# Optimization experiments

Measured on AMD Instinct MI355X. Metric: run time of the kernel, lower is better.

## Reference

```python
import jax, jax.numpy as jnp
import numpy as np

B, T = 32, 2000
H = 512          # hidden_size
NH = 100         # n_harmonics
NM = 65          # n_magnitudes
E = 16           # energy_state dim
HH = 256         # hypernetwork hidden


def _lin_init(k, out_d, in_d):
    return jax.random.normal(k, (out_d, in_d), jnp.float32) / np.sqrt(in_d)


def setup_inputs() -> dict:
    key = jax.random.key(0)
    ks = jax.random.split(key, 24)
    inp = {
        'f0_scaled': jax.random.uniform(ks[0], (B, T), jnp.float32),
        'loudness': jax.random.uniform(ks[1], (B, T), jnp.float32),
        'energy_state': jax.random.normal(ks[2], (B, E), jnp.float32),
        # base decoder params
        'pre_W': _lin_init(ks[3], H, 2), 'pre_b': jnp.zeros((H,), jnp.float32),
        'W_ih': _lin_init(ks[4], 3 * H, H), 'W_hh': _lin_init(ks[5], 3 * H, H),
        'b_ih': jnp.zeros((3 * H,), jnp.float32), 'b_hh': jnp.zeros((3 * H,), jnp.float32),
        'post_W': _lin_init(ks[6], H, H), 'post_b': jnp.zeros((H,), jnp.float32),
        'harm_W': _lin_init(ks[7], NH, H), 'harm_b': jnp.zeros((NH,), jnp.float32),
        'noise_W': _lin_init(ks[8], NM, H), 'noise_b': jnp.zeros((NM,), jnp.float32),
        # hypernetwork params (small output scale so deltas are perturbative)
        'hyp_W1': _lin_init(ks[9], HH, E), 'hyp_b1': jnp.zeros((HH,), jnp.float32),
        'hyp_Wdh': _lin_init(ks[10], NH * H, HH) * 0.05, 'hyp_bdh': jnp.zeros((NH * H,), jnp.float32),
        'hyp_Wbh': _lin_init(ks[11], NH, HH) * 0.05, 'hyp_bbh': jnp.zeros((NH,), jnp.float32),
        'hyp_Wdn': _lin_init(ks[12], NM * H, HH) * 0.05, 'hyp_bdn': jnp.zeros((NM * H,), jnp.float32),
        'hyp_Wbn': _lin_init(ks[13], NM, HH) * 0.05, 'hyp_bbn': jnp.zeros((NM,), jnp.float32),
    }
    return inp


def _gru(x, W_ih, W_hh, b_ih, b_hh):
    # x: [B,T,H] -> [B,T,H], torch nn.GRU cell equations
    gi = jnp.einsum('bth,gh->btg', x, W_ih) + b_ih  # [B,T,3H]
    gi = jnp.swapaxes(gi, 0, 1)  # [T,B,3H]
    h0 = jnp.zeros((x.shape[0], W_hh.shape[1]), x.dtype)

    def step(h, gi_t):
        gh = h @ W_hh.T + b_hh
        ir, iz, in_ = jnp.split(gi_t, 3, axis=-1)
        hr, hz, hn = jnp.split(gh, 3, axis=-1)
        r = jax.nn.sigmoid(ir + hr)
        z = jax.nn.sigmoid(iz + hz)
        n = jnp.tanh(in_ + r * hn)
        h_new = (1.0 - z) * n + z * h
        return h_new, h_new

    _, ys = jax.lax.scan(step, h0, gi)
    return jnp.swapaxes(ys, 0, 1)  # [B,T,H]


def reference(f0_scaled, loudness, energy_state,
              pre_W, pre_b, W_ih, W_hh, b_ih, b_hh, post_W, post_b,
              harm_W, harm_b, noise_W, noise_b,
              hyp_W1, hyp_b1, hyp_Wdh, hyp_bdh, hyp_Wbh, hyp_bbh,
              hyp_Wdn, hyp_bdn, hyp_Wbn, hyp_bbn):
    Bs = energy_state.shape[0]
    # Hypernetwork: energy_state -> per-batch weight/bias deltas
    h = jax.nn.relu(energy_state @ hyp_W1.T + hyp_b1)            # [B,HH]
    dW_harm = (h @ hyp_Wdh.T + hyp_bdh).reshape(Bs, NH, H)
    db_harm = h @ hyp_Wbh.T + hyp_bbh                            # [B,NH]
    dW_noise = (h @ hyp_Wdn.T + hyp_bdn).reshape(Bs, NM, H)
    db_noise = h @ hyp_Wbn.T + hyp_bbn                           # [B,NM]

    # Base decoder trunk
    x = jnp.stack([f0_scaled, loudness], axis=-1)                # [B,T,2]
    x = jax.nn.leaky_relu(jnp.einsum('bti,hi->bth', x, pre_W) + pre_b)
    x = _gru(x, W_ih, W_hh, b_ih, b_hh)
    x = jax.nn.leaky_relu(jnp.einsum('bth,oh->bto', x, post_W) + post_b)

    # Modulated heads: per-batch effective weight shared across T (no [B*T,O,H] blow-up)
    eff_hW = harm_W[None] + dW_harm                              # [B,NH,H]
    eff_hb = harm_b[None] + db_harm                              # [B,NH]
    harm_out = jnp.einsum('bth,boh->bto', x, eff_hW) + eff_hb[:, None, :]
    harmonic_amps = jax.nn.sigmoid(harm_out)                     # [B,T,NH]

    eff_nW = noise_W[None] + dW_noise                            # [B,NM,H]
    eff_nb = noise_b[None] + db_noise                            # [B,NM]
    noise_out = jnp.einsum('bth,boh->bto', x, eff_nW) + eff_nb[:, None, :]
    noise_mags = jax.nn.sigmoid(noise_out)                       # [B,T,NM]
    return harmonic_amps, noise_mags
```

## Files before the change

kernel.cpp:

```cpp
#include <hip/hip_runtime.h>
#include <hip/hip_fp16.h>
#include <stdint.h>

#define B_  32
#define T_  2000
#define H_  512
#define NH_ 100
#define NM_ 65

typedef _Float16 f16x8 __attribute__((ext_vector_type(8)));
typedef _Float16 f16x2 __attribute__((ext_vector_type(2)));
typedef float    f32x4 __attribute__((ext_vector_type(4)));

typedef __attribute__((address_space(3))) void lds_void_t;
typedef __attribute__((address_space(1))) void glb_void_t;

__device__ __forceinline__ void gload_lds16(const void* g, void* l) {
  __builtin_amdgcn_global_load_lds((const glb_void_t*)g, (lds_void_t*)l, 16, 0, 0);
}

__device__ __forceinline__ float sigmoidf_(float x) {
  float e = __builtin_amdgcn_exp2f(-x * 1.44269504f);
  return __builtin_amdgcn_rcpf(1.0f + e);
}
__device__ __forceinline__ float tanhf_(float x) {
  float e = __builtin_amdgcn_exp2f(x * 2.88539008f);
  return 1.0f - 2.0f * __builtin_amdgcn_rcpf(e + 1.0f);
}
__device__ __forceinline__ float dot2(unsigned w, unsigned h, float acc) {
  return __builtin_amdgcn_fdot2(__builtin_bit_cast(f16x2, w),
                                __builtin_bit_cast(f16x2, h), acc, false);
}
__device__ __forceinline__ unsigned pack2(float a, float b) {
  __half2 h = __floats2half2_rn(a, b);
  return __builtin_bit_cast(unsigned, h);
}
__device__ __forceinline__ float hsel(unsigned w, int hi) {
  __half2 h2 = __builtin_bit_cast(__half2, w);
  return hi ? __high2float(h2) : __low2float(h2);
}

__global__ void hyper1(const float* __restrict__ es, const float* __restrict__ W1,
                       const float* __restrict__ b1, float* __restrict__ hE) {
  int b = blockIdx.x, o = threadIdx.x;
  float a = b1[o];
  #pragma unroll
  for (int c = 0; c < 16; ++c) a += es[b*16 + c] * W1[o*16 + c];
  hE[b*256 + o] = fmaxf(a, 0.f);
}

__global__ void hyper2(const float* __restrict__ hE,
                       const float* __restrict__ Wbh, const float* __restrict__ bbh,
                       const float* __restrict__ harmb,
                       const float* __restrict__ Wbn, const float* __restrict__ bbn,
                       const float* __restrict__ noiseb, float* __restrict__ effb) {
  int b = blockIdx.x, o = threadIdx.x;
  if (o < NH_) {
    float a = bbh[o] + harmb[o];
    for (int c = 0; c < 256; ++c) a += hE[b*256 + c] * Wbh[o*256 + c];
    effb[b*256 + o] = a;
  } else if (o < NH_ + NM_) {
    int q = o - NH_;
    float a = bbn[q] + noiseb[q];
    for (int c = 0; c < 256; ++c) a += hE[b*256 + c] * Wbn[q*256 + c];
    effb[b*256 + o] = a;
  }
}

__global__ __launch_bounds__(256) void hyper3(
    const float* __restrict__ hE, const float* __restrict__ Wd,
    const float* __restrict__ bd, const float* __restrict__ baseW,
    __half* __restrict__ effW, int o_base) {
  __shared__ float wl[256*33];
  __shared__ float hEl[32*256];
  int tid = threadIdx.x;
  int row0 = blockIdx.x * 256;
  #pragma unroll
  for (int i = 0; i < 32; ++i) hEl[i*256 + tid] = hE[i*256 + tid];
  float acc[32];
  #pragma unroll
  for (int b = 0; b < 32; ++b) acc[b] = 0.f;
  for (int cc = 0; cc < 256; cc += 32) {
    __syncthreads();
    #pragma unroll
    for (int i = 0; i < 32; ++i) {
      int idx = i*256 + tid;
      int r = idx >> 5, c = idx & 31;
      wl[r*33 + c] = Wd[(size_t)(row0 + r)*256 + cc + c];
    }
    __syncthreads();
    #pragma unroll
    for (int c = 0; c < 32; ++c) {
      float w = wl[tid*33 + c];
      #pragma unroll
      for (int b = 0; b < 32; ++b) acc[b] += w * hEl[b*256 + cc + c];
    }
  }
  int row = row0 + tid;
  int o = row >> 9, h = row & 511;
  float base = baseW[row] + bd[row];
  #pragma unroll
  for (int b = 0; b < 32; ++b) {
    effW[((size_t)b*256 + o_base + o)*512 + h] = (__half)(acc[b] + base);
  }
}

__global__ void cvt_f16(const float* __restrict__ in, __half* __restrict__ out, int n) {
  int i = blockIdx.x*256 + threadIdx.x;
  if (i < n) out[i] = (__half)in[i];
}

__global__ void pack_whh3(const float* __restrict__ Whh, uint4* __restrict__ Wp3) {
  int idx = blockIdx.x*256 + threadIdx.x;
  int t = idx % 384;
  int k = (idx / 384) & 31;
  int w = idx / (384*32);
  int rr = t >> 1, ch = t & 1;
  int g = rr >> 6, j = rr & 63;
  int row = g*512 + w*64 + j;
  int col0 = ch*256 + k*8;
  const float* src = Whh + (size_t)row*512 + col0;
  uint4 o;
  o.x = pack2(src[0], src[1]);
  o.y = pack2(src[2], src[3]);
  o.z = pack2(src[4], src[5]);
  o.w = pack2(src[6], src[7]);
  Wp3[idx] = o;
}

__global__ void pre_kernel(const float* __restrict__ f0, const float* __restrict__ loud,
                           const float* __restrict__ preW, const float* __restrict__ preb,
                           __half* __restrict__ xpre, int CH, int c0) {
  int b = blockIdx.y;
  int idx = blockIdx.x*256 + threadIdx.x;
  int t = idx >> 9, h = idx & 511;
  int mg = b*T_ + c0 + t;
  float v = f0[mg]*preW[h*2+0] + loud[mg]*preW[h*2+1] + preb[h];
  v = v >= 0.f ? v : 0.01f*v;
  xpre[((size_t)b*CH + t)*512 + h] = (__half)v;
}

template<int ACT>
__global__ __launch_bounds__(256) void gemm_nt(
    const __half* __restrict__ A, const __half* __restrict__ B,
    __half* __restrict__ C, const float* __restrict__ bias, int N) {
  constexpr int K = 512;
  __shared__ __align__(16) __half As[128*64];
  __shared__ __align__(16) __half Bs[128*64];
  int tid = threadIdx.x;
  int bx = blockIdx.x, by = blockIdx.y;
  const __half* Ab = A + (size_t)bx*128*K;
  const __half* Bb = B + (size_t)by*128*K;
  f32x4 acc[4][4] = {};
  int lane = tid & 63;
  int wv = tid >> 6, wr = wv >> 1, wc = wv & 1;
  int lr = lane & 15, lk = lane >> 4;

  for (int kt = 0; kt < K/64; ++kt) {
    #pragma unroll
    for (int j = 0; j < 4; ++j) {
      int idx = j*256 + tid;
      int row = idx >> 3, seg = idx & 7;
      const __half* gpA = Ab + (size_t)row*K + kt*64 + seg*8;
      const __half* gpB = Bb + (size_t)row*K + kt*64 + seg*8;
      __half* lpA = As + (size_t)(j*256 + (tid & ~63))*8;
      __half* lpB = Bs + (size_t)(j*256 + (tid & ~63))*8;
      gload_lds16(gpA, lpA);
      gload_lds16(gpB, lpB);
    }
    __syncthreads();
    #pragma unroll
    for (int ks = 0; ks < 2; ++ks) {
      f16x8 af[4], bf[4];
      #pragma unroll
      for (int i = 0; i < 4; ++i)
        af[i] = *(const f16x8*)(As + (wr*64 + i*16 + lr)*64 + ks*32 + lk*8);
      #pragma unroll
      for (int j2 = 0; j2 < 4; ++j2)
        bf[j2] = *(const f16x8*)(Bs + (wc*64 + j2*16 + lr)*64 + ks*32 + lk*8);
      #pragma unroll
      for (int i = 0; i < 4; ++i)
        #pragma unroll
        for (int j2 = 0; j2 < 4; ++j2)
          acc[i][j2] = __builtin_amdgcn_mfma_f32_16x16x32_f16(af[i], bf[j2], acc[i][j2], 0, 0, 0);
    }
    __syncthreads();
  }

  #pragma unroll
  for (int j2 = 0; j2 < 4; ++j2) {
    int col = by*128 + wc*64 + j2*16 + lr;
    float bv = bias[col];
    #pragma unroll
    for (int i = 0; i < 4; ++i) {
      int row0 = bx*128 + wr*64 + i*16 + lk*4;
      #pragma unroll
      for (int r = 0; r < 4; ++r) {
        float v = acc[i][j2][r] + bv;
        if (ACT == 1) v = v >= 0.f ? v : 0.01f*v;
        C[(size_t)(row0 + r)*N + col] = (__half)v;
      }
    }
  }
}

__global__ __launch_bounds__(256) void heads_gemm(
    const __half* __restrict__ Apc, const __half* __restrict__ effW,
    const float* __restrict__ effb, float* __restrict__ out, int CH, int c0) {
  constexpr int K = 512;
  __shared__ __align__(16) __half As[128*64];
  __shared__ __align__(16) __half Bs[128*64];
  int tid = threadIdx.x;
  int bx = blockIdx.x, by = blockIdx.y, b = blockIdx.z;
  const __half* Ab = Apc + (size_t)b*CH*K;
  const __half* Bb = effW + ((size_t)b*256 + (size_t)by*128)*K;
  f32x4 acc[4][4] = {};
  int lane = tid & 63;
  int wv = tid >> 6, wr = wv >> 1, wc = wv & 1;
  int lr = lane & 15, lk = lane >> 4;

  for (int kt = 0; kt < K/64; ++kt) {
    #pragma unroll
    for (int j = 0; j < 4; ++j) {
      int idx = j*256 + tid;
      int row = idx >> 3, seg = idx & 7;
      int ar = bx*128 + row; if (ar > CH-1) ar = CH-1;
      const __half* gpA = Ab + (size_t)ar*K + kt*64 + seg*8;
      const __half* gpB = Bb + (size_t)row*K + kt*64 + seg*8;
      __half* lpA = As + (size_t)(j*256 + (tid & ~63))*8;
      __half* lpB = Bs + (size_t)(j*256 + (tid & ~63))*8;
      gload_lds16(gpA, lpA);
      gload_lds16(gpB, lpB);
    }
    __syncthreads();
    #pragma unroll
    for (int ks = 0; ks < 2; ++ks) {
      f16x8 af[4], bf[4];
      #pragma unroll
      for (int i = 0; i < 4; ++i)
        af[i] = *(const f16x8*)(As + (wr*64 + i*16 + lr)*64 + ks*32 + lk*8);
      #pragma unroll
      for (int j2 = 0; j2 < 4; ++j2)
        bf[j2] = *(const f16x8*)(Bs + (wc*64 + j2*16 + lr)*64 + ks*32 + lk*8);
      #pragma unroll
      for (int i = 0; i < 4; ++i)
        #pragma unroll
        for (int j2 = 0; j2 < 4; ++j2)
          acc[i][j2] = __builtin_amdgcn_mfma_f32_16x16x32_f16(af[i], bf[j2], acc[i][j2], 0, 0, 0);
    }
    __syncthreads();
  }

  #pragma unroll
  for (int j2 = 0; j2 < 4; ++j2) {
    int o = by*128 + wc*64 + j2*16 + lr;
    if (o < NH_ + NM_) {
      float bv = effb[b*256 + o];
      #pragma unroll
      for (int i = 0; i < 4; ++i) {
        #pragma unroll
        for (int r = 0; r < 4; ++r) {
          int trow = bx*128 + wr*64 + i*16 + lk*4 + r;
          if (trow < CH) {
            int tg = c0 + trow;
            float v = sigmoidf_(acc[i][j2][r] + bv);
            if (o < NH_)
              out[((size_t)b*T_ + tg)*NH_ + o] = v;
            else
              out[(size_t)B_*T_*NH_ + ((size_t)b*T_ + tg)*NM_ + (o - NH_)] = v;
          }
        }
      }
    }
  }
}

#define LOADW(k) { const uint4* p = Wp3 + ((size_t)(w*32 + (k)))*384 + t; \
  asm volatile("global_load_dwordx4 %0, %1, off" : "=v"(wq_##k) : "v"(p) : "memory"); }

#define DOTW(k, A) { uint4 hv = *(const uint4*)&hq[ch*132 + (k)*4]; \
  A = dot2(wq_##k.x, hv.x, A); A = dot2(wq_##k.y, hv.y, A); \
  A = dot2(wq_##k.z, hv.z, A); A = dot2(wq_##k.w, hv.w, A); }

__global__ __launch_bounds__(512) __attribute__((amdgpu_waves_per_eu(2, 4)))
void gru_scan8(
    const uint4* __restrict__ Wp3, const __half* __restrict__ gi_c,
    const float* __restrict__ bhh, __half* __restrict__ ys_c,
    float* __restrict__ hstate, unsigned long long* __restrict__ xch64,
    int CH, int first) {
  int wg = blockIdx.x;
  int b = wg & 31;
  int w = wg >> 5;
  int t = threadIdx.x;
  int rr = t >> 1, ch = t & 1;
  bool wact = (t < 384);

  __shared__ __align__(16) unsigned hq[264];
  __shared__ float part[384];
  __shared__ float gil[192];
  __shared__ unsigned sval[32];

  uint4 wq_0{},wq_1{},wq_2{},wq_3{},wq_4{},wq_5{},wq_6{},wq_7{},
        wq_8{},wq_9{},wq_10{},wq_11{},wq_12{},wq_13{},wq_14{},wq_15{},
        wq_16{},wq_17{},wq_18{},wq_19{},wq_20{},wq_21{},wq_22{},wq_23{},
        wq_24{},wq_25{},wq_26{},wq_27{},wq_28{},wq_29{},wq_30{},wq_31{};
  if (wact) {
    LOADW(0)  LOADW(1)  LOADW(2)  LOADW(3)  LOADW(4)  LOADW(5)  LOADW(6)  LOADW(7)
    LOADW(8)  LOADW(9)  LOADW(10) LOADW(11) LOADW(12) LOADW(13) LOADW(14) LOADW(15)
    LOADW(16) LOADW(17) LOADW(18) LOADW(19) LOADW(20) LOADW(21) LOADW(22) LOADW(23)
    LOADW(24) LOADW(25) LOADW(26) LOADW(27) LOADW(28) LOADW(29) LOADW(30) LOADW(31)
  }
  asm volatile("s_waitcnt vmcnt(0)" ::: "memory");
  __builtin_amdgcn_sched_barrier(0);

  float br0=0.f,br1=0.f,bz0=0.f,bz1=0.f,bn0=0.f,bn1=0.f;
  if (t < 32) {
    int u0 = w*64 + 2*t;
    br0 = bhh[u0];        br1 = bhh[u0+1];
    bz0 = bhh[512+u0];    bz1 = bhh[512+u0+1];
    bn0 = bhh[1024+u0];   bn1 = bhh[1024+u0+1];
  }

  if (t < 256) {
    unsigned hv0 = first ? 0u : pack2(hstate[b*512 + 2*t], hstate[b*512 + 2*t + 1]);
    hq[t < 128 ? t : t + 4] = hv0;
  }
  __syncthreads();

  const __half* gib = gi_c + (size_t)b*CH*1536;
  __half* ysb = ys_c + (size_t)b*CH*512;

  for (int s = 0; s < CH; ++s) {
    int p = s & 1;
    unsigned long long* xp64 = xch64 + ((size_t)p*32 + b)*256;
    float giv = 0.f;
    if (t < 192) giv = (float)gib[(size_t)s*1536 + (t >> 6)*512 + w*64 + (t & 63)];

    if (wact) {
      float a0 = 0.f, a1 = 0.f, a2 = 0.f, a3 = 0.f;
      DOTW(0,a0)  DOTW(1,a1)  DOTW(2,a2)  DOTW(3,a3)
      DOTW(4,a0)  DOTW(5,a1)  DOTW(6,a2)  DOTW(7,a3)
      DOTW(8,a0)  DOTW(9,a1)  DOTW(10,a2) DOTW(11,a3)
      DOTW(12,a0) DOTW(13,a1) DOTW(14,a2) DOTW(15,a3)
      DOTW(16,a0) DOTW(17,a1) DOTW(18,a2) DOTW(19,a3)
      DOTW(20,a0) DOTW(21,a1) DOTW(22,a2) DOTW(23,a3)
      DOTW(24,a0) DOTW(25,a1) DOTW(26,a2) DOTW(27,a3)
      DOTW(28,a0) DOTW(29,a1) DOTW(30,a2) DOTW(31,a3)
      part[rr*2 + ch] = (a0 + a1) + (a2 + a3);
      if (t < 192) gil[t] = giv;
    }
    __syncthreads();

    if (t < 32) {
      int j0 = 2*t, j1 = 2*t + 1;
      float ghr0 = part[j0*2] + part[j0*2+1] + br0;
      float ghr1 = part[j1*2] + part[j1*2+1] + br1;
      float ghz0 = part[(64+j0)*2] + part[(64+j0)*2+1] + bz0;
      float ghz1 = part[(64+j1)*2] + part[(64+j1)*2+1] + bz1;
      float ghn0 = part[(128+j0)*2] + part[(128+j0)*2+1] + bn0;
      float ghn1 = part[(128+j1)*2] + part[(128+j1)*2+1] + bn1;
      float r0 = sigmoidf_(gil[j0] + ghr0);
      float r1 = sigmoidf_(gil[j1] + ghr1);
      float z0 = sigmoidf_(gil[64+j0] + ghz0);
      float z1 = sigmoidf_(gil[64+j1] + ghz1);
      float n0 = tanhf_(gil[128+j0] + r0*ghn0);
      float n1 = tanhf_(gil[128+j1] + r1*ghn1);
      int gidx = w*32 + t;
      unsigned hold = hq[gidx < 128 ? gidx : gidx + 4];
      float h0 = (1.f - z0)*n0 + z0*hsel(hold, 0);
      float h1 = (1.f - z1)*n1 + z1*hsel(hold, 1);
      unsigned hv = pack2(h0, h1);
      *(unsigned*)&ysb[(size_t)s*512 + w*64 + j0] = hv;
      unsigned long long tv = ((unsigned long long)(unsigned)(s + 1) << 32)
                              | (unsigned long long)hv;
      __hip_atomic_store(&xp64[w*32 + t], tv,
                         __ATOMIC_RELAXED, __HIP_MEMORY_SCOPE_AGENT);
      sval[t] = hv;
      if (s == CH - 1) {
        hstate[b*512 + w*64 + j0] = h0;
        hstate[b*512 + w*64 + j1] = h1;
      }
    }
    __syncthreads();
    if (t < 256) {
      unsigned hv;
      if ((t >> 5) == w) {
        hv = sval[t & 31];
      } else {
        unsigned long long v;
        do {
          v = __hip_atomic_load(&xp64[t], __ATOMIC_RELAXED, __HIP_MEMORY_SCOPE_AGENT);
        } while ((unsigned)(v >> 32) != (unsigned)(s + 1));
        hv = (unsigned)v;
      }
      hq[t < 128 ? t : t + 4] = hv;
    }
    __syncthreads();
  }
}

extern "C" void kernel_launch(void* const* d_in, const int* in_sizes, int n_in,
                              void* d_out, int out_size, void* d_ws, size_t ws_size,
                              hipStream_t stream) {
  const float* f0     = (const float*)d_in[0];
  const float* loud   = (const float*)d_in[1];
  const float* es     = (const float*)d_in[2];
  const float* preW   = (const float*)d_in[3];
  const float* preb   = (const float*)d_in[4];
  const float* Wih    = (const float*)d_in[5];
  const float* Whh    = (const float*)d_in[6];
  const float* b_ih   = (const float*)d_in[7];
  const float* b_hh   = (const float*)d_in[8];
  const float* postW  = (const float*)d_in[9];
  const float* postb  = (const float*)d_in[10];
  const float* harmW  = (const float*)d_in[11];
  const float* harmb  = (const float*)d_in[12];
  const float* noiseW = (const float*)d_in[13];
  const float* noiseb = (const float*)d_in[14];
  const float* hypW1  = (const float*)d_in[15];
  const float* hypb1  = (const float*)d_in[16];
  const float* Wdh    = (const float*)d_in[17];
  const float* bdh    = (const float*)d_in[18];
  const float* Wbh    = (const float*)d_in[19];
  const float* bbh    = (const float*)d_in[20];
  const float* Wdn    = (const float*)d_in[21];
  const float* bdn    = (const float*)d_in[22];
  const float* Wbn    = (const float*)d_in[23];
  const float* bbn    = (const float*)d_in[24];
  (void)in_sizes; (void)n_in; (void)out_size;

  const size_t FIXED = 13312ull*1024ull;
  int CH = 20;
  {
    const int opts[8] = {2000, 1000, 500, 400, 200, 100, 40, 20};
    for (int i = 0; i < 8; ++i) {
      size_t need = FIXED + (size_t)opts[i] * 163840ull + 65536ull;
      if (need <= ws_size) { CH = opts[i]; break; }
    }
  }
  const int NC = T_ / CH;
  const int Mc = B_ * CH;

  char* w = (char*)d_ws;
  size_t off = 0;
  auto alloc = [&](size_t bytes) -> void* {
    void* p = (void*)(w + off);
    off += (bytes + 255) & ~(size_t)255;
    return p;
  };
  float*    hE      = (float*)alloc((size_t)32*256*4);
  float*    effb    = (float*)alloc((size_t)32*256*4);
  float*    hstate  = (float*)alloc((size_t)32*512*4);
  __half*   effW    = (__half*)alloc((size_t)32*256*512*2);
  __half*   Wih16   = (__half*)alloc((size_t)1536*512*2);
  __half*   postW16 = (__half*)alloc((size_t)512*512*2);
  uint4*    Wp3     = (uint4*)alloc((size_t)8*32*384*16 + 4096);
  unsigned long long* xch64 = (unsigned long long*)alloc((size_t)2*32*256*8);
  __half*   xpre    = (__half*)alloc((size_t)Mc*512*2);
  __half*   gibuf   = (__half*)alloc((size_t)Mc*1536*2);
  __half*   ysbuf   = (__half*)alloc((size_t)Mc*512*2);
  __half*   postc   = xpre;

  hyper1<<<32, 256, 0, stream>>>(es, hypW1, hypb1, hE);
  hyper2<<<32, 256, 0, stream>>>(hE, Wbh, bbh, harmb, Wbn, bbn, noiseb, effb);
  hyper3<<<200, 256, 0, stream>>>(hE, Wdh, bdh, harmW, effW, 0);
  hyper3<<<130, 256, 0, stream>>>(hE, Wdn, bdn, noiseW, effW, NH_);
  cvt_f16<<<(1536*512)/256, 256, 0, stream>>>(Wih, Wih16, 1536*512);
  cvt_f16<<<(512*512)/256, 256, 0, stream>>>(postW, postW16, 512*512);
  pack_whh3<<<384, 256, 0, stream>>>(Whh, Wp3);

  for (int c = 0; c < NC; ++c) {
    int c0 = c * CH;
    pre_kernel<<<dim3(CH*2, 32), 256, 0, stream>>>(f0, loud, preW, preb, xpre, CH, c0);
    gemm_nt<0><<<dim3(Mc/128, 12), 256, 0, stream>>>(xpre, Wih16, gibuf, b_ih, 1536);
    gru_scan8<<<256, 512, 0, stream>>>(Wp3, gibuf, b_hh, ysbuf, hstate, xch64,
                                       CH, c == 0 ? 1 : 0);
    gemm_nt<1><<<dim3(Mc/128, 4), 256, 0, stream>>>(ysbuf, postW16, postc, postb, 512);
    heads_gemm<<<dim3((CH+127)/128, 2, 32), 256, 0, stream>>>(postc, effW, effb,
                                                              (float*)d_out, CH, c0);
  }
}
```

Measured before the change: 4.512 ms.

## Move GRU gate combine to idle wave and cut per-step barriers

The gate-combine step moves from threads 0-31 to an otherwise idle wave (threads 384-415). That wave writes its own new hidden slice straight into hq, while the other threads spin-poll for remote slices at the same time. This removes one of the three block barriers per timestep, and the remaining barriers become raw s_barrier with an lgkmcnt wait. The gi load for the next step is also prefetched one iteration ahead. The change adds a data race risk, because hq is written while other lanes may still read it, and the hand-written barrier depends on correct waitcnt handling.

```diff
diff --git a/kernel.cpp b/kernel.cpp
--- a/kernel.cpp
+++ b/kernel.cpp
@@ -282,6 +282,9 @@
   A = dot2(wq_##k.x, hv.x, A); A = dot2(wq_##k.y, hv.y, A); \
   A = dot2(wq_##k.z, hv.z, A); A = dot2(wq_##k.w, hv.w, A); }
 
+#define BARX() do { asm volatile("s_waitcnt lgkmcnt(0)\n\ts_barrier" ::: "memory"); \
+                    __builtin_amdgcn_sched_barrier(0); } while (0)
+
 __global__ __launch_bounds__(512) __attribute__((amdgpu_waves_per_eu(2, 4)))
 void gru_scan8(
     const uint4* __restrict__ Wp3, const __half* __restrict__ gi_c,
@@ -292,13 +295,14 @@
   int b = wg & 31;
   int w = wg >> 5;
   int t = threadIdx.x;
-  int rr = t >> 1, ch = t & 1;
+  int ch = t & 1;
   bool wact = (t < 384);
+  bool comb = (t >= 384 && t < 416);
+  int tc = t - 384;
 
   __shared__ __align__(16) unsigned hq[264];
   __shared__ float part[384];
   __shared__ float gil[192];
-  __shared__ unsigned sval[32];
 
   uint4 wq_0{},wq_1{},wq_2{},wq_3{},wq_4{},wq_5{},wq_6{},wq_7{},
         wq_8{},wq_9{},wq_10{},wq_11{},wq_12{},wq_13{},wq_14{},wq_15{},
@@ -314,8 +318,8 @@
   __builtin_amdgcn_sched_barrier(0);
 
   float br0=0.f,br1=0.f,bz0=0.f,bz1=0.f,bn0=0.f,bn1=0.f;
-  if (t < 32) {
-    int u0 = w*64 + 2*t;
+  if (comb) {
+    int u0 = w*64 + 2*tc;
     br0 = bhh[u0];        br1 = bhh[u0+1];
     bz0 = bhh[512+u0];    bz1 = bhh[512+u0+1];
     bn0 = bhh[1024+u0];   bn1 = bhh[1024+u0+1];
@@ -330,11 +334,15 @@
   const __half* gib = gi_c + (size_t)b*CH*1536;
   __half* ysb = ys_c + (size_t)b*CH*512;
 
+  float giv_cur = 0.f, giv_next = 0.f;
+  if (t < 192) giv_cur = (float)gib[(t >> 6)*512 + w*64 + (t & 63)];
+
   for (int s = 0; s < CH; ++s) {
     int p = s & 1;
     unsigned long long* xp64 = xch64 + ((size_t)p*32 + b)*256;
-    float giv = 0.f;
-    if (t < 192) giv = (float)gib[(size_t)s*1536 + (t >> 6)*512 + w*64 + (t & 63)];
+
+    if (t < 192 && s + 1 < CH)
+      giv_next = (float)gib[(size_t)(s+1)*1536 + (t >> 6)*512 + w*64 + (t & 63)];
 
     if (wact) {
       float a0 = 0.f, a1 = 0.f, a2 = 0.f, a3 = 0.f;
@@ -346,13 +354,14 @@
       DOTW(20,a0) DOTW(21,a1) DOTW(22,a2) DOTW(23,a3)
       DOTW(24,a0) DOTW(25,a1) DOTW(26,a2) DOTW(27,a3)
       DOTW(28,a0) DOTW(29,a1) DOTW(30,a2) DOTW(31,a3)
-      part[rr*2 + ch] = (a0 + a1) + (a2 + a3);
-      if (t < 192) gil[t] = giv;
-    }
-    __syncthreads();
-
-    if (t < 32) {
-      int j0 = 2*t, j1 = 2*t + 1;
+      part[t] = (a0 + a1) + (a2 + a3);
+      if (t < 192) gil[t] = giv_cur;
+    }
+    giv_cur = giv_next;
+    BARX();
+
+    if (comb) {
+      int j0 = 2*tc, j1 = 2*tc + 1;
       float ghr0 = part[j0*2] + part[j0*2+1] + br0;
       float ghr1 = part[j1*2] + part[j1*2+1] + br1;
       float ghz0 = part[(64+j0)*2] + part[(64+j0)*2+1] + bz0;
@@ -365,37 +374,30 @@
       float z1 = sigmoidf_(gil[64+j1] + ghz1);
       float n0 = tanhf_(gil[128+j0] + r0*ghn0);
       float n1 = tanhf_(gil[128+j1] + r1*ghn1);
-      int gidx = w*32 + t;
-      unsigned hold = hq[gidx < 128 ? gidx : gidx + 4];
+      int gidx = w*32 + tc;
+      int hidx = gidx < 128 ? gidx : gidx + 4;
+      unsigned hold = hq[hidx];
       float h0 = (1.f - z0)*n0 + z0*hsel(hold, 0);
       float h1 = (1.f - z1)*n1 + z1*hsel(hold, 1);
       unsigned hv = pack2(h0, h1);
+      hq[hidx] = hv;
       *(unsigned*)&ysb[(size_t)s*512 + w*64 + j0] = hv;
       unsigned long long tv = ((unsigned long long)(unsigned)(s + 1) << 32)
                               | (unsigned long long)hv;
-      __hip_atomic_store(&xp64[w*32 + t], tv,
+      __hip_atomic_store(&xp64[gidx], tv,
                          __ATOMIC_RELAXED, __HIP_MEMORY_SCOPE_AGENT);
-      sval[t] = hv;
       if (s == CH - 1) {
         hstate[b*512 + w*64 + j0] = h0;
         hstate[b*512 + w*64 + j1] = h1;
       }
-    }
-    __syncthreads();
-    if (t < 256) {
-      unsigned hv;
-      if ((t >> 5) == w) {
-        hv = sval[t & 31];
-      } else {
-        unsigned long long v;
-        do {
-          v = __hip_atomic_load(&xp64[t], __ATOMIC_RELAXED, __HIP_MEMORY_SCOPE_AGENT);
-        } while ((unsigned)(v >> 32) != (unsigned)(s + 1));
-        hv = (unsigned)v;
-      }
-      hq[t < 128 ? t : t + 4] = hv;
-    }
-    __syncthreads();
+    } else if (t < 256 && (t >> 5) != w) {
+      unsigned long long v;
+      do {
+        v = __hip_atomic_load(&xp64[t], __ATOMIC_RELAXED, __HIP_MEMORY_SCOPE_AGENT);
+      } while ((unsigned)(v >> 32) != (unsigned)(s + 1));
+      hq[t < 128 ? t : t + 4] = (unsigned)v;
+    }
+    BARX();
   }
 }
 
```

Result: slower. 4.630 ms (+2.6%).
